# Kernel tuning notes

Hardware: AMD Instinct MI355X
Metric: run time of the kernel (lower is better)

Reference implementation:

```python
import jax, jax.numpy as jnp
import numpy as np

CHEB_K = 2  # chebyshev polynomial order (support_ks = [I, A] for cheb_k=2)


def _fc(x, w1, b1, w2, b2, w3, b3):
    # FC module: Linear -> sigmoid -> Linear -> sigmoid -> Linear
    h = jax.nn.sigmoid(x @ w1 + b1)
    h = jax.nn.sigmoid(h @ w2 + b2)
    return h @ w3 + b3


def _preprocess(adj):
    # adj: [B,N,N]; add self-loops then row-normalize
    adj = adj + jnp.eye(adj.shape[-1], dtype=adj.dtype)
    return adj / adj.sum(-1, keepdims=True)


def _gcn(x, adjs, ne, wpool, bpool):
    # x: [B,N,C], adjs: list of [B,N,N], ne: [N,E]
    # wpool: [E, 2*CHEB_K, C, O], bpool: [E, O]
    mats = []
    for A in adjs:
        ks = [jnp.broadcast_to(jnp.eye(A.shape[-1], dtype=A.dtype), A.shape), A]
        for _ in range(2, CHEB_K):
            ks.append(2.0 * jnp.matmul(A, ks[-1]) - ks[-2])
        mats.extend(ks)
    # [B,N,K,C] with K = 2*CHEB_K
    x_g = jnp.stack([jnp.einsum('bnm,bmc->bnc', S, x) for S in mats], axis=2)
    weights = jnp.einsum('nd,dkio->nkio', ne, wpool)  # [N,K,C,O]
    bias = ne @ bpool  # [N,O]
    return jnp.einsum('bnki,nkio->bno', x_g, weights) + bias


def _forward(x, state, ne0, ne1, ne2, fc1_w1, fc1_b1, fc1_w2, fc1_b2, fc1_w3, fc1_b3,
             fc2_w1, fc2_b1, fc2_w2, fc2_b2, fc2_w3, fc2_b3, gate_w, gate_b, upd_w, upd_b):
    hid = upd_w.shape[-1]
    ins = jnp.concatenate([x, state], axis=-1)  # [B,N,dim_in+hid]
    f1 = _fc(ins, fc1_w1, fc1_b1, fc1_w2, fc1_b2, fc1_w3, fc1_b3)  # [B,N,TD]
    f2 = _fc(ins, fc2_w1, fc2_b1, fc2_w2, fc2_b2, fc2_w3, fc2_b3)
    nv1 = jnp.tanh(ne0[:, None, :] * f1)  # einsum 'bd,bnd->bnd' == broadcast mul
    nv2 = jnp.tanh(ne1[:, None, :] * f2)
    adj = jnp.einsum('bnd,bmd->bnm', nv1, nv2) - jnp.einsum('bnd,bmd->bnm', nv2, nv1)
    adj1 = _preprocess(jax.nn.relu(adj))
    adj2 = _preprocess(jax.nn.relu(-jnp.swapaxes(adj, -2, -1)))
    z_r = jax.nn.sigmoid(_gcn(ins, [adj1, adj2], ne2, gate_w, gate_b))
    z, r = z_r[..., :hid], z_r[..., hid:]
    cand = jnp.concatenate([x, z * state], axis=-1)
    hc = jnp.tanh(_gcn(cand, [adj1, adj2], ne2, upd_w, upd_b))
    return r * state + (1.0 - r) * hc


def setup_inputs():
    B, N, DIN, DOUT, ED, TD = 32, 1024, 2, 64, 10, 32
    HG, MID = 16, 2  # hyperGNN_dim, middle_dim hardcoded in FC
    CIN = DIN + DOUT
    K2 = 2 * CHEB_K
    ks = jax.random.split(jax.random.key(0), 16)
    rn = lambda i, shape, s=1.0: jax.random.normal(ks[i], shape, dtype=jnp.float32) * s
    return {
        'x': rn(0, (B, N, DIN)),
        'state': rn(1, (B, N, DOUT)),
        'ne0': rn(2, (B, TD)),
        'ne1': rn(3, (B, TD)),
        'ne2': rn(4, (N, ED), 0.1),
        'fc1_w1': rn(5, (CIN, HG), 0.1), 'fc1_b1': jnp.zeros((HG,), jnp.float32),
        'fc1_w2': rn(6, (HG, MID), 0.1), 'fc1_b2': jnp.zeros((MID,), jnp.float32),
        'fc1_w3': rn(7, (MID, TD), 0.1), 'fc1_b3': jnp.zeros((TD,), jnp.float32),
        'fc2_w1': rn(8, (CIN, HG), 0.1), 'fc2_b1': jnp.zeros((HG,), jnp.float32),
        'fc2_w2': rn(9, (HG, MID), 0.1), 'fc2_b2': jnp.zeros((MID,), jnp.float32),
        'fc2_w3': rn(10, (MID, TD), 0.1), 'fc2_b3': jnp.zeros((TD,), jnp.float32),
        'gate_w': rn(11, (ED, K2, CIN, 2 * DOUT), 0.1),
        'gate_b': rn(12, (ED, 2 * DOUT), 0.1),
        'upd_w': rn(13, (ED, K2, CIN, DOUT), 0.1),
        'upd_b': rn(14, (ED, DOUT), 0.1),
    }


def reference(x, state, ne0, ne1, ne2, fc1_w1, fc1_b1, fc1_w2, fc1_b2, fc1_w3, fc1_b3,
              fc2_w1, fc2_b1, fc2_w2, fc2_b2, fc2_w3, fc2_b3, gate_w, gate_b, upd_w, upd_b):
    return _forward(x, state, ne0, ne1, ne2, fc1_w1, fc1_b1, fc1_w2, fc1_b2, fc1_w3, fc1_b3,
                    fc2_w1, fc2_b1, fc2_w2, fc2_b2, fc2_w3, fc2_b3, gate_w, gate_b, upd_w, upd_b)
```

## Files before the change

kernel.cpp:

```cpp
#include <hip/hip_runtime.h>
#include <math.h>

#define BB   32
#define NN   1024
#define DIN  2
#define DOUT 64
#define CIN  66
#define TD   32
#define ED   10
#define OG   128
#define OU   64
#define KP   160
#define XTR  80

typedef __bf16 bf16x8 __attribute__((ext_vector_type(8)));
typedef float  f32x4  __attribute__((ext_vector_type(4)));
typedef short  s16x8  __attribute__((ext_vector_type(8)));

__device__ __forceinline__ unsigned short f2b(float f) {
    __bf16 h = (__bf16)f;
    return *(unsigned short*)&h;
}

__device__ __forceinline__ unsigned int cvt_pk_bf16(float lo, float hi) {
    unsigned int r;
    asm("v_cvt_pk_bf16_f32 %0, %1, %2" : "=v"(r) : "v"(lo), "v"(hi));
    return r;
}
__device__ __forceinline__ void perm32swap(unsigned int& a, unsigned int& b) {
    asm("v_permlane32_swap_b32 %0, %1" : "+v"(a), "+v"(b));
}
__device__ __forceinline__ void perm16swap(unsigned int& a, unsigned int& b) {
    asm("v_permlane16_swap_b32 %0, %1" : "+v"(a), "+v"(b));
}

__global__ __launch_bounds__(256) void k_pre(
    const float* __restrict__ x, const float* __restrict__ state,
    const float* __restrict__ ne0, const float* __restrict__ ne1,
    const float* __restrict__ ne2,
    const float* __restrict__ w11, const float* __restrict__ b11,
    const float* __restrict__ w12, const float* __restrict__ b12,
    const float* __restrict__ w13, const float* __restrict__ b13,
    const float* __restrict__ w21, const float* __restrict__ b21,
    const float* __restrict__ w22, const float* __restrict__ b22,
    const float* __restrict__ w23, const float* __restrict__ b23,
    const float* __restrict__ gate_w, const float* __restrict__ gate_b,
    const float* __restrict__ upd_w, const float* __restrict__ upd_b,
    unsigned short* __restrict__ nv1b, unsigned short* __restrict__ nv2b,
    unsigned short* __restrict__ XT0, unsigned short* __restrict__ XT1,
    unsigned short* __restrict__ BcTg, unsigned short* __restrict__ BcTu,
    float* __restrict__ biasG, float* __restrict__ biasU)
{
    __shared__ float sw[2408];
    __shared__ unsigned short st[68*72];
    int blk = blockIdx.x;
    int t = threadIdx.x;

    if (blk < 128) {
        const int oW1 = 0, oB1 = 1056, oW2 = 1072, oB2 = 1104, oW3 = 1108, oB3 = 1172, F2 = 1204;
        for (int i = t; i < 1056; i += 256) { sw[oW1+i] = w11[i]; sw[F2+oW1+i] = w21[i]; }
        if (t < 16) { sw[oB1+t] = b11[t]; sw[F2+oB1+t] = b21[t]; }
        if (t < 32) { sw[oW2+t] = w12[t]; sw[F2+oW2+t] = w22[t]; }
        if (t < 2)  { sw[oB2+t] = b12[t]; sw[F2+oB2+t] = b22[t]; }
        if (t < 64) { sw[oW3+t] = w13[t]; sw[F2+oW3+t] = w23[t]; }
        if (t >= 64 && t < 96) { sw[oB3+t-64] = b13[t-64]; sw[F2+oB3+t-64] = b23[t-64]; }
        __syncthreads();

        int p = blk*256 + t;
        int b = p >> 10;

        float h1a[16], h1b[16];
        #pragma unroll
        for (int j = 0; j < 16; ++j) { h1a[j] = sw[oB1+j]; h1b[j] = sw[F2+oB1+j]; }
        for (int i = 0; i < CIN; ++i) {
            float v = (i < DIN) ? x[(size_t)p*DIN + i] : state[(size_t)p*DOUT + (i-DIN)];
            #pragma unroll
            for (int jq = 0; jq < 4; ++jq) {
                float4 wa = *(const float4*)&sw[oW1 + i*16 + jq*4];
                float4 wb = *(const float4*)&sw[F2 + oW1 + i*16 + jq*4];
                h1a[jq*4+0] += v*wa.x; h1a[jq*4+1] += v*wa.y;
                h1a[jq*4+2] += v*wa.z; h1a[jq*4+3] += v*wa.w;
                h1b[jq*4+0] += v*wb.x; h1b[jq*4+1] += v*wb.y;
                h1b[jq*4+2] += v*wb.z; h1b[jq*4+3] += v*wb.w;
            }
        }
        #pragma unroll
        for (int j = 0; j < 16; ++j) {
            h1a[j] = 1.f/(1.f + __expf(-h1a[j]));
            h1b[j] = 1.f/(1.f + __expf(-h1b[j]));
        }
        float h2a0 = sw[oB2+0], h2a1 = sw[oB2+1];
        float h2b0 = sw[F2+oB2+0], h2b1 = sw[F2+oB2+1];
        #pragma unroll
        for (int i = 0; i < 16; ++i) {
            h2a0 += h1a[i]*sw[oW2 + i*2 + 0];
            h2a1 += h1a[i]*sw[oW2 + i*2 + 1];
            h2b0 += h1b[i]*sw[F2+oW2 + i*2 + 0];
            h2b1 += h1b[i]*sw[F2+oW2 + i*2 + 1];
        }
        h2a0 = 1.f/(1.f + __expf(-h2a0)); h2a1 = 1.f/(1.f + __expf(-h2a1));
        h2b0 = 1.f/(1.f + __expf(-h2b0)); h2b1 = 1.f/(1.f + __expf(-h2b1));

        const float* pn0 = ne0 + b*TD;
        const float* pn1 = ne1 + b*TD;
        #pragma unroll
        for (int jq = 0; jq < 8; ++jq) {
            float4 ba  = *(const float4*)&sw[oB3 + jq*4];
            float4 wa0 = *(const float4*)&sw[oW3 + jq*4];
            float4 wa1 = *(const float4*)&sw[oW3 + 32 + jq*4];
            float4 bb2 = *(const float4*)&sw[F2+oB3 + jq*4];
            float4 wb0 = *(const float4*)&sw[F2+oW3 + jq*4];
            float4 wb1 = *(const float4*)&sw[F2+oW3 + 32 + jq*4];
            float4 n0 = *(const float4*)&pn0[jq*4];
            float4 n1 = *(const float4*)&pn1[jq*4];
            ushort4 u1, u2;
            u1.x = f2b(tanhf(n0.x*(ba.x + h2a0*wa0.x + h2a1*wa1.x)));
            u1.y = f2b(tanhf(n0.y*(ba.y + h2a0*wa0.y + h2a1*wa1.y)));
            u1.z = f2b(tanhf(n0.z*(ba.z + h2a0*wa0.z + h2a1*wa1.z)));
            u1.w = f2b(tanhf(n0.w*(ba.w + h2a0*wa0.w + h2a1*wa1.w)));
            u2.x = f2b(tanhf(n1.x*(bb2.x + h2b0*wb0.x + h2b1*wb1.x)));
            u2.y = f2b(tanhf(n1.y*(bb2.y + h2b0*wb0.y + h2b1*wb1.y)));
            u2.z = f2b(tanhf(n1.z*(bb2.z + h2b0*wb0.z + h2b1*wb1.z)));
            u2.w = f2b(tanhf(n1.w*(bb2.w + h2b0*wb0.w + h2b1*wb1.w)));
            *(ushort4*)&nv1b[(size_t)p*TD + jq*4] = u1;
            *(ushort4*)&nv2b[(size_t)p*TD + jq*4] = u2;
        }
    } else if (blk < 640) {
        int idx = blk - 128;
        int b = idx >> 4, m0 = (idx & 15)*64;
        for (int i = t; i < 1024; i += 256) {
            int m = i >> 4, cq = i & 15;
            size_t base = (size_t)b*NN + m0 + m;
            float4 v = *(const float4*)&state[base*DOUT + cq*4];
            st[(2 + cq*4 + 0)*72 + m] = f2b(v.x);
            st[(2 + cq*4 + 1)*72 + m] = f2b(v.y);
            st[(2 + cq*4 + 2)*72 + m] = f2b(v.z);
            st[(2 + cq*4 + 3)*72 + m] = f2b(v.w);
        }
        if (t < 128) {
            int m = t >> 1, c = t & 1;
            st[c*72 + m] = f2b(x[((size_t)b*NN + m0 + m)*DIN + c]);
        }
        __syncthreads();
        const unsigned int ONE2 = 0x3F803F80u;
        for (int i = t; i < XTR*8; i += 256) {
            int c = i >> 3, ch = i & 7;
            uint4 v;
            if (c < 66)      v = *(const uint4*)&st[c*72 + ch*8];
            else if (c == 66) v = make_uint4(ONE2, ONE2, ONE2, ONE2);
            else              v = make_uint4(0, 0, 0, 0);
            *(uint4*)&XT0[((size_t)b*XTR + c)*NN + m0 + ch*8] = v;
            if (c < 2 || c >= 66)
                *(uint4*)&XT1[((size_t)b*XTR + c)*NN + m0 + ch*8] = v;
        }
    } else if (blk < 1840) {
        int tid = (blk - 640)*256 + t;
        int c = tid / KP, k = tid - c*KP;
        const float* pool; int O, cc; unsigned short* dst;
        if (c < 1280) { pool = gate_w; O = OG; cc = c;        dst = BcTg; }
        else          { pool = upd_w;  O = OU; cc = c - 1280; dst = BcTu; }
        int d = cc / O, o = cc - d*O;
        float v = 0.f;
        if (k < 132) {
            int kp = (k < 66) ? 0 : 1;
            int i  = (k < 66) ? k : k - 66;
            v = pool[(size_t)((d*4 + kp)*CIN + i)*O + o]
              + pool[(size_t)((d*4 + kp + 2)*CIN + i)*O + o];
        }
        dst[(size_t)cc*KP + k] = f2b(v);
    } else {
        int i = (blk - 1840)*256 + t;
        int n = i / 192, j = i - n*192;
        float v = 0.f;
        if (j < 128) {
            #pragma unroll
            for (int d = 0; d < ED; ++d) v += ne2[(size_t)n*ED + d]*gate_b[d*OG + j];
            biasG[(size_t)n*OG + j] = v;
        } else {
            int o = j - 128;
            #pragma unroll
            for (int d = 0; d < ED; ++d) v += ne2[(size_t)n*ED + d]*upd_b[d*OU + o];
            biasU[(size_t)n*OU + o] = v;
        }
    }
}

__global__ __launch_bounds__(256) void k_aapply(
    const unsigned short* __restrict__ nv1b, const unsigned short* __restrict__ nv2b,
    const unsigned short* __restrict__ XTg, unsigned short* __restrict__ A)
{
    __shared__ unsigned short s_nv1c[2][2560];
    __shared__ unsigned short s_nv2c[2][2560];
    __shared__ unsigned short s_xt[2][5760];

    int t = threadIdx.x;
    int id = blockIdx.x;
    int b = id & 31, rbase = (id >> 5)*64;
    int w = t >> 6, lane = t & 63, lq = lane >> 4, ln = lane & 15;

    bf16x8 a1 = *(const bf16x8*)&nv1b[((size_t)b*NN + rbase + 16*w + ln)*TD + lq*8];
    s16x8 a2s = *(const s16x8*)&nv2b[((size_t)b*NN + rbase + 16*w + ln)*TD + lq*8];
    const s16x8 sgn = {(short)0x8000,(short)0x8000,(short)0x8000,(short)0x8000,
                       (short)0x8000,(short)0x8000,(short)0x8000,(short)0x8000};
    a2s ^= sgn;
    bf16x8 a2n = (bf16x8)a2s;

    const unsigned short* pnv1 = nv1b + (size_t)b*NN*TD;
    const unsigned short* pnv2 = nv2b + (size_t)b*NN*TD;
    const unsigned short* pxt  = XTg  + (size_t)b*XTR*NN;
    int nnode = t >> 2;
    int nch   = (t & 3)*8;
    int xc    = t >> 3;
    int xch   = (t & 7)*8;

    uint4 q0, q1, r0, r1, r2;

    f32x4 acc[5];
    #pragma unroll
    for (int k = 0; k < 5; ++k) acc[k] = (f32x4){0.f,0.f,0.f,0.f};
    const f32x4 zero4 = {0.f,0.f,0.f,0.f};
    union U8 { unsigned int u[4]; bf16x8 v; };

    q0 = *(const uint4*)&pnv1[(size_t)nnode*TD + nch];
    q1 = *(const uint4*)&pnv2[(size_t)nnode*TD + nch];
    r0 = *(const uint4*)&pxt[(size_t)xc*NN + xch];
    r1 = *(const uint4*)&pxt[(size_t)(xc+32)*NN + xch];
    if (t < 128) r2 = *(const uint4*)&pxt[(size_t)(xc+64)*NN + xch];
    *(uint4*)&s_nv1c[0][nnode*40 + nch] = q0;
    *(uint4*)&s_nv2c[0][nnode*40 + nch] = q1;
    *(uint4*)&s_xt[0][xc*72 + xch] = r0;
    *(uint4*)&s_xt[0][(xc+32)*72 + xch] = r1;
    if (t < 128) *(uint4*)&s_xt[0][(xc+64)*72 + xch] = r2;
    q0 = *(const uint4*)&pnv1[(size_t)(64 + nnode)*TD + nch];
    q1 = *(const uint4*)&pnv2[(size_t)(64 + nnode)*TD + nch];
    r0 = *(const uint4*)&pxt[(size_t)xc*NN + 64 + xch];
    r1 = *(const uint4*)&pxt[(size_t)(xc+32)*NN + 64 + xch];
    if (t < 128) r2 = *(const uint4*)&pxt[(size_t)(xc+64)*NN + 64 + xch];
    __syncthreads();

    int cur = 0;
    for (int mb = 0; mb < NN; mb += 64) {
        if (mb + 64 < NN) {
            *(uint4*)&s_nv1c[cur^1][nnode*40 + nch] = q0;
            *(uint4*)&s_nv2c[cur^1][nnode*40 + nch] = q1;
            *(uint4*)&s_xt[cur^1][xc*72 + xch] = r0;
            *(uint4*)&s_xt[cur^1][(xc+32)*72 + xch] = r1;
            if (t < 128) *(uint4*)&s_xt[cur^1][(xc+64)*72 + xch] = r2;
        }
        if (mb + 128 < NN) {
            int mb2 = mb + 128;
            q0 = *(const uint4*)&pnv1[(size_t)(mb2 + nnode)*TD + nch];
            q1 = *(const uint4*)&pnv2[(size_t)(mb2 + nnode)*TD + nch];
            r0 = *(const uint4*)&pxt[(size_t)xc*NN + mb2 + xch];
            r1 = *(const uint4*)&pxt[(size_t)(xc+32)*NN + mb2 + xch];
            if (t < 128) r2 = *(const uint4*)&pxt[(size_t)(xc+64)*NN + mb2 + xch];
        }

        unsigned int u[4][2];
        #pragma unroll
        for (int jj = 0; jj < 4; ++jj) {
            bf16x8 b2 = *(const bf16x8*)&s_nv2c[cur][(jj*16 + ln)*40 + lq*8];
            bf16x8 b1 = *(const bf16x8*)&s_nv1c[cur][(jj*16 + ln)*40 + lq*8];
            f32x4 s = __builtin_amdgcn_mfma_f32_16x16x32_bf16(b2, a1,  zero4, 0, 0, 0);
            s       = __builtin_amdgcn_mfma_f32_16x16x32_bf16(b1, a2n, s,     0, 0, 0);
            u[jj][0] = cvt_pk_bf16(fmaxf(s[0], 0.f), fmaxf(s[1], 0.f));
            u[jj][1] = cvt_pk_bf16(fmaxf(s[2], 0.f), fmaxf(s[3], 0.f));
        }

        unsigned int w00 = u[0][0], w20 = u[1][0]; perm32swap(w00, w20); perm16swap(w00, w20);
        unsigned int w01 = u[0][1], w21 = u[1][1]; perm32swap(w01, w21); perm16swap(w01, w21);
        unsigned int x00 = u[2][0], x20 = u[3][0]; perm32swap(x00, x20); perm16swap(x00, x20);
        unsigned int x01 = u[2][1], x21 = u[3][1]; perm32swap(x01, x21); perm16swap(x01, x21);
        U8 p0, p1;
        p0.u[0] = w00; p0.u[1] = w01; p0.u[2] = w20; p0.u[3] = w21;
        p1.u[0] = x00; p1.u[1] = x01; p1.u[2] = x20; p1.u[3] = x21;
        bf16x8 pa0 = p0.v, pa1 = p1.v;

        #pragma unroll
        for (int k = 0; k < 5; ++k) {
            bf16x8 xb0 = *(const bf16x8*)&s_xt[cur][(k*16 + ln)*72 +      lq*8];
            bf16x8 xb1 = *(const bf16x8*)&s_xt[cur][(k*16 + ln)*72 + 32 + lq*8];
            acc[k] = __builtin_amdgcn_mfma_f32_16x16x32_bf16(pa0, xb0, acc[k], 0, 0, 0);
            acc[k] = __builtin_amdgcn_mfma_f32_16x16x32_bf16(pa1, xb1, acc[k], 0, 0, 0);
        }

        __syncthreads();
        cur ^= 1;
    }

    float rinv[4];
    #pragma unroll
    for (int r = 0; r < 4; ++r) {
        float rs = __shfl(acc[4][r], (lane & 48) | 2, 64);
        rinv[r] = 1.0f / (1.0f + rs);
    }

    #pragma unroll
    for (int k = 0; k < 5; ++k) {
        int c = k*16 + ln;
        if (c < CIN) {
            #pragma unroll
            for (int r = 0; r < 4; ++r) {
                int gr = rbase + 16*w + lq*4 + r;
                size_t rowG = (size_t)b*NN + gr;
                unsigned short xu = XTg[((size_t)b*XTR + c)*NN + gr];
                float xr = (float)(*(const __bf16*)&xu);
                A[rowG*KP + c]      = xu;
                A[rowG*KP + 66 + c] = f2b((acc[k][r] + xr) * rinv[r]);
            }
        }
    }
    for (int i = t; i < 64*28; i += 256) {
        int rr = i / 28, cc = 132 + (i - 28*(i/28));
        A[((size_t)b*NN + rbase + rr)*KP + cc] = 0;
    }
}

template<int O, int MODE>
__global__ __launch_bounds__(256) void k_gemm(
    const unsigned short* __restrict__ A, const unsigned short* __restrict__ BcT,
    const float* __restrict__ ne2, const float* __restrict__ biasP,
    const float* __restrict__ state, unsigned short* __restrict__ XT1,
    float* __restrict__ rbuf, float* __restrict__ out)
{
    __shared__ unsigned short s_b[80*168];

    int t = threadIdx.x;
    int w = t >> 6, lane = t & 63, lq = lane >> 4, ln = lane & 15;
    int o0 = blockIdx.y*16;
    int rowBlock = blockIdx.x*128;
    int rowW = rowBlock + w*32;
    int o = o0 + ln;

    float part[2][4];
    f32x4 acc[2][5];

    #pragma unroll
    for (int h = 0; h < 2; ++h) {
        if (h) __syncthreads();
        for (int i = t; i < 1600; i += 256) {
            int cc = i / 20, kc = i - cc*20;
            int d = h*5 + (cc >> 4), oo = cc & 15;
            *(uint4*)&s_b[cc*168 + kc*8] =
                *(const uint4*)&BcT[(size_t)(d*O + o0 + oo)*KP + kc*8];
        }
        #pragma unroll
        for (int f = 0; f < 2; ++f)
            #pragma unroll
            for (int c = 0; c < 5; ++c) acc[f][c] = (f32x4){0.f,0.f,0.f,0.f};
        __syncthreads();

        #pragma unroll
        for (int kc = 0; kc < 5; ++kc) {
            bf16x8 af0 = *(const bf16x8*)&A[(size_t)(rowW      + ln)*KP + kc*32 + lq*8];
            bf16x8 af1 = *(const bf16x8*)&A[(size_t)(rowW + 16 + ln)*KP + kc*32 + lq*8];
            #pragma unroll
            for (int ct = 0; ct < 5; ++ct) {
                bf16x8 bf = *(const bf16x8*)&s_b[(ct*16 + ln)*168 + kc*32 + lq*8];
                acc[0][ct] = __builtin_amdgcn_mfma_f32_16x16x32_bf16(af0, bf, acc[0][ct], 0, 0, 0);
                acc[1][ct] = __builtin_amdgcn_mfma_f32_16x16x32_bf16(af1, bf, acc[1][ct], 0, 0, 0);
            }
        }

        #pragma unroll
        for (int f = 0; f < 2; ++f) {
            #pragma unroll
            for (int r = 0; r < 4; ++r) {
                int row_l = w*32 + 16*f + lq*4 + r;
                size_t rowG = (size_t)rowBlock + row_l;
                int n = (int)(rowG & (NN - 1));
                const float* nep = &ne2[(size_t)n*ED];
                float val = (h == 0) ? biasP[(size_t)n*O + o] : part[f][r];
                #pragma unroll
                for (int d = 0; d < 5; ++d) val += nep[h*5 + d] * acc[f][d][r];
                if (h == 0) {
                    part[f][r] = val;
                } else {
                    int bb = (int)(rowG >> 10);
                    if (MODE == 0) {
                        float sv = 1.f/(1.f + __expf(-val));
                        if (o < 64) {
                            float zst = sv * state[rowG*DOUT + o];
                            XT1[((size_t)bb*XTR + 2 + o)*NN + n] = f2b(zst);
                        } else {
                            rbuf[rowG*DOUT + (o - 64)] = sv;
                        }
                    } else {
                        float hc = tanhf(val);
                        float rg = rbuf[rowG*DOUT + o];
                        float st = state[rowG*DOUT + o];
                        out[rowG*DOUT + o] = rg*st + (1.f - rg)*hc;
                    }
                }
            }
        }
    }
}

extern "C" void kernel_launch(void* const* d_in, const int* in_sizes, int n_in,
                              void* d_out, int out_size, void* d_ws, size_t ws_size,
                              hipStream_t stream)
{
    const float* x      = (const float*)d_in[0];
    const float* state  = (const float*)d_in[1];
    const float* ne0    = (const float*)d_in[2];
    const float* ne1    = (const float*)d_in[3];
    const float* ne2    = (const float*)d_in[4];
    const float* f1w1   = (const float*)d_in[5];
    const float* f1b1   = (const float*)d_in[6];
    const float* f1w2   = (const float*)d_in[7];
    const float* f1b2   = (const float*)d_in[8];
    const float* f1w3   = (const float*)d_in[9];
    const float* f1b3   = (const float*)d_in[10];
    const float* f2w1   = (const float*)d_in[11];
    const float* f2b1   = (const float*)d_in[12];
    const float* f2w2   = (const float*)d_in[13];
    const float* f2b2   = (const float*)d_in[14];
    const float* f2w3   = (const float*)d_in[15];
    const float* f2b3   = (const float*)d_in[16];
    const float* gate_w = (const float*)d_in[17];
    const float* gate_b = (const float*)d_in[18];
    const float* upd_w  = (const float*)d_in[19];
    const float* upd_b  = (const float*)d_in[20];

    unsigned short* nv1b = (unsigned short*)d_ws;
    unsigned short* nv2b = nv1b + (size_t)BB*NN*TD;
    unsigned short* XT0  = nv2b + (size_t)BB*NN*TD;
    unsigned short* XT1  = XT0  + (size_t)BB*XTR*NN;
    unsigned short* A    = XT1  + (size_t)BB*XTR*NN;
    unsigned short* BcTg = A    + (size_t)BB*NN*KP;
    unsigned short* BcTu = BcTg + (size_t)1280*KP;
    float* biasG = (float*)(BcTu + (size_t)640*KP);
    float* biasU = biasG + (size_t)NN*OG;
    float* rbuf  = biasU + (size_t)NN*OU;
    float* out   = (float*)d_out;

    k_pre<<<dim3(2608), 256, 0, stream>>>(x, state, ne0, ne1, ne2,
        f1w1, f1b1, f1w2, f1b2, f1w3, f1b3,
        f2w1, f2b1, f2w2, f2b2, f2w3, f2b3,
        gate_w, gate_b, upd_w, upd_b,
        nv1b, nv2b, XT0, XT1, BcTg, BcTu, biasG, biasU);

    k_aapply<<<dim3(512), 256, 0, stream>>>(nv1b, nv2b, XT0, A);

    k_gemm<OG,0><<<dim3(BB*NN/128, 8), 256, 0, stream>>>(A, BcTg, ne2, biasG,
                                                         state, XT1, rbuf, nullptr);

    k_aapply<<<dim3(512), 256, 0, stream>>>(nv1b, nv2b, XT1, A);

    k_gemm<OU,1><<<dim3(BB*NN/128, 4), 256, 0, stream>>>(A, BcTu, ne2, biasU,
                                                         state, nullptr, rbuf, out);
}
```

Measured before the change: 228.9 us.

## Fuse adjacency-apply and weight GEMM into one kernel via shared-memory A tile

Merges k_aapply and k_gemm into a single templated kernel. The 64-row aggregated activation tile stays in LDS instead of round-tripping through a global A buffer, and each block then loops over all output tiles, reloading BcT slices into shared memory. This removes the global write and read of A and two launches. In exchange, only 512 blocks each do the full output loop serially, with more barriers and BcT reloads per block, so the GEMM stage gets less parallelism.

```diff
diff --git a/kernel.cpp b/kernel.cpp
--- a/kernel.cpp
+++ b/kernel.cpp
@@ -185,13 +185,18 @@
     }
 }
 
-__global__ __launch_bounds__(256) void k_aapply(
+template<int O, int MODE>
+__global__ __launch_bounds__(256) void k_fused(
     const unsigned short* __restrict__ nv1b, const unsigned short* __restrict__ nv2b,
-    const unsigned short* __restrict__ XTg, unsigned short* __restrict__ A)
+    const unsigned short* __restrict__ XTg, const unsigned short* __restrict__ BcT,
+    const float* __restrict__ ne2, const float* __restrict__ biasP,
+    const float* __restrict__ state, unsigned short* __restrict__ XT1,
+    float* __restrict__ rbuf, float* __restrict__ out)
 {
-    __shared__ unsigned short s_nv1c[2][2560];
-    __shared__ unsigned short s_nv2c[2][2560];
-    __shared__ unsigned short s_xt[2][5760];
+    __shared__ unsigned short smem[24192];
+    unsigned short* s_nv1c = smem;
+    unsigned short* s_nv2c = smem + 5120;
+    unsigned short* s_xt   = smem + 10240;
 
     int t = threadIdx.x;
     int id = blockIdx.x;
@@ -226,11 +231,11 @@
     r0 = *(const uint4*)&pxt[(size_t)xc*NN + xch];
     r1 = *(const uint4*)&pxt[(size_t)(xc+32)*NN + xch];
     if (t < 128) r2 = *(const uint4*)&pxt[(size_t)(xc+64)*NN + xch];
-    *(uint4*)&s_nv1c[0][nnode*40 + nch] = q0;
-    *(uint4*)&s_nv2c[0][nnode*40 + nch] = q1;
-    *(uint4*)&s_xt[0][xc*72 + xch] = r0;
-    *(uint4*)&s_xt[0][(xc+32)*72 + xch] = r1;
-    if (t < 128) *(uint4*)&s_xt[0][(xc+64)*72 + xch] = r2;
+    *(uint4*)&s_nv1c[nnode*40 + nch] = q0;
+    *(uint4*)&s_nv2c[nnode*40 + nch] = q1;
+    *(uint4*)&s_xt[xc*72 + xch] = r0;
+    *(uint4*)&s_xt[(xc+32)*72 + xch] = r1;
+    if (t < 128) *(uint4*)&s_xt[(xc+64)*72 + xch] = r2;
     q0 = *(const uint4*)&pnv1[(size_t)(64 + nnode)*TD + nch];
     q1 = *(const uint4*)&pnv2[(size_t)(64 + nnode)*TD + nch];
     r0 = *(const uint4*)&pxt[(size_t)xc*NN + 64 + xch];
@@ -241,11 +246,12 @@
     int cur = 0;
     for (int mb = 0; mb < NN; mb += 64) {
         if (mb + 64 < NN) {
-            *(uint4*)&s_nv1c[cur^1][nnode*40 + nch] = q0;
-            *(uint4*)&s_nv2c[cur^1][nnode*40 + nch] = q1;
-            *(uint4*)&s_xt[cur^1][xc*72 + xch] = r0;
-            *(uint4*)&s_xt[cur^1][(xc+32)*72 + xch] = r1;
-            if (t < 128) *(uint4*)&s_xt[cur^1][(xc+64)*72 + xch] = r2;
+            int nx = cur ^ 1;
+            *(uint4*)&s_nv1c[nx*2560 + nnode*40 + nch] = q0;
+            *(uint4*)&s_nv2c[nx*2560 + nnode*40 + nch] = q1;
+            *(uint4*)&s_xt[nx*5760 + xc*72 + xch] = r0;
+            *(uint4*)&s_xt[nx*5760 + (xc+32)*72 + xch] = r1;
+            if (t < 128) *(uint4*)&s_xt[nx*5760 + (xc+64)*72 + xch] = r2;
         }
         if (mb + 128 < NN) {
             int mb2 = mb + 128;
@@ -259,8 +265,8 @@
         unsigned int u[4][2];
         #pragma unroll
         for (int jj = 0; jj < 4; ++jj) {
-            bf16x8 b2 = *(const bf16x8*)&s_nv2c[cur][(jj*16 + ln)*40 + lq*8];
-            bf16x8 b1 = *(const bf16x8*)&s_nv1c[cur][(jj*16 + ln)*40 + lq*8];
+            bf16x8 b2 = *(const bf16x8*)&s_nv2c[cur*2560 + (jj*16 + ln)*40 + lq*8];
+            bf16x8 b1 = *(const bf16x8*)&s_nv1c[cur*2560 + (jj*16 + ln)*40 + lq*8];
             f32x4 s = __builtin_amdgcn_mfma_f32_16x16x32_bf16(b2, a1,  zero4, 0, 0, 0);
             s       = __builtin_amdgcn_mfma_f32_16x16x32_bf16(b1, a2n, s,     0, 0, 0);
             u[jj][0] = cvt_pk_bf16(fmaxf(s[0], 0.f), fmaxf(s[1], 0.f));
@@ -278,8 +284,8 @@
 
         #pragma unroll
         for (int k = 0; k < 5; ++k) {
-            bf16x8 xb0 = *(const bf16x8*)&s_xt[cur][(k*16 + ln)*72 +      lq*8];
-            bf16x8 xb1 = *(const bf16x8*)&s_xt[cur][(k*16 + ln)*72 + 32 + lq*8];
+            bf16x8 xb0 = *(const bf16x8*)&s_xt[cur*5760 + (k*16 + ln)*72 +      lq*8];
+            bf16x8 xb1 = *(const bf16x8*)&s_xt[cur*5760 + (k*16 + ln)*72 + 32 + lq*8];
             acc[k] = __builtin_amdgcn_mfma_f32_16x16x32_bf16(pa0, xb0, acc[k], 0, 0, 0);
             acc[k] = __builtin_amdgcn_mfma_f32_16x16x32_bf16(pa1, xb1, acc[k], 0, 0, 0);
         }
@@ -295,93 +301,74 @@
         rinv[r] = 1.0f / (1.0f + rs);
     }
 
+    unsigned short* s_A = smem;
+    unsigned short* s_B = smem + 10752;
+
+    for (int i = t; i < 64*28; i += 256) {
+        int rr = i / 28, cc = 132 + (i - 28*(i/28));
+        s_A[rr*168 + cc] = 0;
+    }
     #pragma unroll
     for (int k = 0; k < 5; ++k) {
         int c = k*16 + ln;
         if (c < CIN) {
             #pragma unroll
             for (int r = 0; r < 4; ++r) {
-                int gr = rbase + 16*w + lq*4 + r;
-                size_t rowG = (size_t)b*NN + gr;
+                int row_l = 16*w + lq*4 + r;
+                int gr = rbase + row_l;
                 unsigned short xu = XTg[((size_t)b*XTR + c)*NN + gr];
                 float xr = (float)(*(const __bf16*)&xu);
-                A[rowG*KP + c]      = xu;
-                A[rowG*KP + 66 + c] = f2b((acc[k][r] + xr) * rinv[r]);
+                s_A[row_l*168 + c]      = xu;
+                s_A[row_l*168 + 66 + c] = f2b((acc[k][r] + xr) * rinv[r]);
             }
         }
     }
-    for (int i = t; i < 64*28; i += 256) {
-        int rr = i / 28, cc = 132 + (i - 28*(i/28));
-        A[((size_t)b*NN + rbase + rr)*KP + cc] = 0;
-    }
-}
-
-template<int O, int MODE>
-__global__ __launch_bounds__(256) void k_gemm(
-    const unsigned short* __restrict__ A, const unsigned short* __restrict__ BcT,
-    const float* __restrict__ ne2, const float* __restrict__ biasP,
-    const float* __restrict__ state, unsigned short* __restrict__ XT1,
-    float* __restrict__ rbuf, float* __restrict__ out)
-{
-    __shared__ unsigned short s_b[80*168];
-
-    int t = threadIdx.x;
-    int w = t >> 6, lane = t & 63, lq = lane >> 4, ln = lane & 15;
-    int o0 = blockIdx.y*16;
-    int rowBlock = blockIdx.x*128;
-    int rowW = rowBlock + w*32;
-    int o = o0 + ln;
-
-    float part[2][4];
-    f32x4 acc[2][5];
-
-    #pragma unroll
-    for (int h = 0; h < 2; ++h) {
-        if (h) __syncthreads();
-        for (int i = t; i < 1600; i += 256) {
-            int cc = i / 20, kc = i - cc*20;
-            int d = h*5 + (cc >> 4), oo = cc & 15;
-            *(uint4*)&s_b[cc*168 + kc*8] =
-                *(const uint4*)&BcT[(size_t)(d*O + o0 + oo)*KP + kc*8];
-        }
-        #pragma unroll
-        for (int f = 0; f < 2; ++f)
-            #pragma unroll
-            for (int c = 0; c < 5; ++c) acc[f][c] = (f32x4){0.f,0.f,0.f,0.f};
-        __syncthreads();
-
-        #pragma unroll
-        for (int kc = 0; kc < 5; ++kc) {
-            bf16x8 af0 = *(const bf16x8*)&A[(size_t)(rowW      + ln)*KP + kc*32 + lq*8];
-            bf16x8 af1 = *(const bf16x8*)&A[(size_t)(rowW + 16 + ln)*KP + kc*32 + lq*8];
-            #pragma unroll
-            for (int ct = 0; ct < 5; ++ct) {
-                bf16x8 bf = *(const bf16x8*)&s_b[(ct*16 + ln)*168 + kc*32 + lq*8];
-                acc[0][ct] = __builtin_amdgcn_mfma_f32_16x16x32_bf16(af0, bf, acc[0][ct], 0, 0, 0);
-                acc[1][ct] = __builtin_amdgcn_mfma_f32_16x16x32_bf16(af1, bf, acc[1][ct], 0, 0, 0);
+
+    for (int ot = 0; ot < O/16; ++ot) {
+        int o0 = ot*16, o = o0 + ln;
+        float part[4];
+        f32x4 gac[5];
+
+        #pragma unroll
+        for (int h = 0; h < 2; ++h) {
+            __syncthreads();
+            for (int i = t; i < 1600; i += 256) {
+                int cc = i / 20, kc = i - cc*20;
+                int d = h*5 + (cc >> 4), oo = cc & 15;
+                *(uint4*)&s_B[cc*168 + kc*8] =
+                    *(const uint4*)&BcT[(size_t)(d*O + o0 + oo)*KP + kc*8];
             }
-        }
-
-        #pragma unroll
-        for (int f = 0; f < 2; ++f) {
+            #pragma unroll
+            for (int c = 0; c < 5; ++c) gac[c] = (f32x4){0.f,0.f,0.f,0.f};
+            __syncthreads();
+
+            #pragma unroll
+            for (int kc = 0; kc < 5; ++kc) {
+                bf16x8 af = *(const bf16x8*)&s_A[(16*w + ln)*168 + kc*32 + lq*8];
+                #pragma unroll
+                for (int ct = 0; ct < 5; ++ct) {
+                    bf16x8 bf = *(const bf16x8*)&s_B[(ct*16 + ln)*168 + kc*32 + lq*8];
+                    gac[ct] = __builtin_amdgcn_mfma_f32_16x16x32_bf16(af, bf, gac[ct], 0, 0, 0);
+                }
+            }
+
             #pragma unroll
             for (int r = 0; r < 4; ++r) {
-                int row_l = w*32 + 16*f + lq*4 + r;
-                size_t rowG = (size_t)rowBlock + row_l;
-                int n = (int)(rowG & (NN - 1));
+                int row_l = 16*w + lq*4 + r;
+                int n = rbase + row_l;
+                size_t rowG = (size_t)b*NN + n;
                 const float* nep = &ne2[(size_t)n*ED];
-                float val = (h == 0) ? biasP[(size_t)n*O + o] : part[f][r];
+                float val = (h == 0) ? biasP[(size_t)n*O + o] : part[r];
                 #pragma unroll
-                for (int d = 0; d < 5; ++d) val += nep[h*5 + d] * acc[f][d][r];
+                for (int d = 0; d < 5; ++d) val += nep[h*5 + d] * gac[d][r];
                 if (h == 0) {
-                    part[f][r] = val;
+                    part[r] = val;
                 } else {
-                    int bb = (int)(rowG >> 10);
                     if (MODE == 0) {
                         float sv = 1.f/(1.f + __expf(-val));
                         if (o < 64) {
                             float zst = sv * state[rowG*DOUT + o];
-                            XT1[((size_t)bb*XTR + 2 + o)*NN + n] = f2b(zst);
+                            XT1[((size_t)b*XTR + 2 + o)*NN + n] = f2b(zst);
                         } else {
                             rbuf[rowG*DOUT + (o - 64)] = sv;
                         }
@@ -427,8 +414,7 @@
     unsigned short* nv2b = nv1b + (size_t)BB*NN*TD;
     unsigned short* XT0  = nv2b + (size_t)BB*NN*TD;
     unsigned short* XT1  = XT0  + (size_t)BB*XTR*NN;
-    unsigned short* A    = XT1  + (size_t)BB*XTR*NN;
-    unsigned short* BcTg = A    + (size_t)BB*NN*KP;
+    unsigned short* BcTg = XT1  + (size_t)BB*XTR*NN;
     unsigned short* BcTu = BcTg + (size_t)1280*KP;
     float* biasG = (float*)(BcTu + (size_t)640*KP);
     float* biasU = biasG + (size_t)NN*OG;
@@ -441,13 +427,9 @@
         gate_w, gate_b, upd_w, upd_b,
         nv1b, nv2b, XT0, XT1, BcTg, BcTu, biasG, biasU);
 
-    k_aapply<<<dim3(512), 256, 0, stream>>>(nv1b, nv2b, XT0, A);
-
-    k_gemm<OG,0><<<dim3(BB*NN/128, 8), 256, 0, stream>>>(A, BcTg, ne2, biasG,
-                                                         state, XT1, rbuf, nullptr);
-
-    k_aapply<<<dim3(512), 256, 0, stream>>>(nv1b, nv2b, XT1, A);
-
-    k_gemm<OU,1><<<dim3(BB*NN/128, 4), 256, 0, stream>>>(A, BcTu, ne2, biasU,
-                                                         state, nullptr, rbuf, out);
-}
+    k_fused<OG,0><<<dim3(512), 256, 0, stream>>>(nv1b, nv2b, XT0, BcTg, ne2,
+                                                 biasG, state, XT1, rbuf, nullptr);
+
+    k_fused<OU,1><<<dim3(512), 256, 0, stream>>>(nv1b, nv2b, XT1, BcTu, ne2,
+                                                 biasU, state, nullptr, rbuf, out);
+}
```

Result: no change. 230.3 us (+0.6%).
